# Kernel optimization log

Hardware: AMD Instinct MI355X
Metric: run time of the kernel (lower is better)

Reference implementation:

```python
import jax, jax.numpy as jnp
import numpy as np

H, B, D, C = 6, 512, 2048, 1000   # heads (5 ICs + backbone exit), batch, feat dim, classes
TAU = 0.5                          # confidence_threshold


def setup_inputs() -> dict:
    key = jax.random.key(0)
    k1, k2, k3, k4 = jax.random.split(key, 4)
    feats = jax.random.normal(k1, (H, B, D), dtype=jnp.float32)          # pooled reps at each exit
    W = jax.random.normal(k2, (H, D, C), dtype=jnp.float32) * 0.07       # per-head classifier weights
    b = jax.random.normal(k3, (H, C), dtype=jnp.float32) * 0.1
    y_true = jax.random.randint(k4, (B,), 0, C)
    return {"feats": feats, "W": W, "b": b, "y_true": y_true}


def reference(feats, W, b, y_true):
    # Per-head logits for every sample (vectorized replacement for the shrinking-batch loop).
    logits = jnp.einsum('hbd,hdc->hbc', feats, W) + b[:, None, :]        # [H, B, C]
    logp = jax.nn.log_softmax(logits, axis=-1)
    conf = jnp.exp(logp).max(axis=-1)                                    # [H, B] max softmax prob (prob_conf=True)

    # Early-exit routing: first head with conf >= TAU; else head with max confidence
    # (argmax returns the first occurrence, matching the strict '>' update in find_exit).
    exited = conf >= TAU                                                  # [H, B]
    any_exit = exited.any(axis=0)                                         # [B]
    first_exit = jnp.argmax(exited, axis=0)                               # [B] first True along heads
    best_conf = jnp.argmax(conf, axis=0)                                  # [B] fallback exit
    exit_idx = jnp.where(any_exit, first_exit, best_conf)                 # [B] == sample_exited_at

    # Gather the chosen head's logits per sample (vectorized masked-scatter of sample_outputs).
    outputs = jnp.take_along_axis(logits, exit_idx[None, :, None], axis=0)[0]   # [B, C]

    # criterion_ic: cross-entropy loss + accuracy on routed outputs
    out_logp = jax.nn.log_softmax(outputs, axis=-1)
    loss = -jnp.take_along_axis(out_logp, y_true[:, None], axis=1).mean()
    acc = (outputs.argmax(axis=-1) == y_true).astype(jnp.float32).mean()
    return outputs, exit_idx.astype(jnp.int32), loss, acc
```

## Files before the change

kernel.cpp:

```cpp
#include <hip/hip_runtime.h>
#include <math.h>

#define Hn 6
#define Bn 512
#define Dn 2048
#define Cn 1000
#define Cpad 1024
#define TAUv 0.5f
#define KSPLIT 4
#define KPER (Dn / KSPLIT)
#define KT 32
#define NIT (KPER / KT)
#define NKT (Dn / KT)

typedef unsigned int u32;
typedef unsigned short u16;
typedef __attribute__((ext_vector_type(8))) short short8;
typedef __attribute__((ext_vector_type(4))) float f32x4;

union FragU { u32 d[4]; short8 s; };

__device__ __forceinline__ u32 bf16_rne(float f) {
  const u32 u = __float_as_uint(f);
  return (u + 0x7FFFu + ((u >> 16) & 1u)) >> 16;
}
__device__ __forceinline__ u32 pack_rne2(float f0, float f1, float& r0, float& r1) {
  const u32 b0 = bf16_rne(f0), b1 = bf16_rne(f1);
  r0 = f0 - __uint_as_float(b0 << 16);
  r1 = f1 - __uint_as_float(b1 << 16);
  return b0 | (b1 << 16);
}

__device__ __forceinline__ void dma16(const void* g, void* l) {
  __builtin_amdgcn_global_load_lds(
      (const __attribute__((address_space(1))) u32*)g,
      (__attribute__((address_space(3))) u32*)l, 16, 0, 0);
}

__device__ __forceinline__ void pack8(const float* rr, uint4& hv, uint4& lv) {
  float x0, x1, x2, x3, y0, y1, y2, y3, d;
  hv.x = pack_rne2(rr[0], rr[1], x0, x1);
  hv.y = pack_rne2(rr[2], rr[3], x2, x3);
  hv.z = pack_rne2(rr[4], rr[5], y0, y1);
  hv.w = pack_rne2(rr[6], rr[7], y2, y3);
  lv.x = pack_rne2(x0, x1, d, d);
  lv.y = pack_rne2(x2, x3, d, d);
  lv.z = pack_rne2(y0, y1, d, d);
  lv.w = pack_rne2(y2, y3, d, d);
}

__global__ __launch_bounds__(256) void aconv_k(const float* __restrict__ feats,
                                               u16* __restrict__ Ah, u16* __restrict__ Al)
{
  const int t  = blockIdx.x;
  const int rg = blockIdx.y;
  const int h  = blockIdx.z;
  const int r0 = rg * 128;
  __shared__ float tile[128][33];
  const int tid = threadIdx.x;

#pragma unroll
  for (int i = 0; i < 4; ++i) {
    const int f = i * 256 + tid;
    const int r = f >> 3, q = f & 7;
    const float4 v = *(const float4*)(feats + ((size_t)(h * Bn + r0 + r) * Dn + t * 32 + q * 4));
    tile[r][q * 4 + 0] = v.x; tile[r][q * 4 + 1] = v.y;
    tile[r][q * 4 + 2] = v.z; tile[r][q * 4 + 3] = v.w;
  }
  __syncthreads();
#pragma unroll
  for (int i = 0; i < 2; ++i) {
    const int j = i * 256 + tid;
    const int c = j >> 7, r = j & 127;
    float rr[8];
#pragma unroll
    for (int e = 0; e < 8; ++e) rr[e] = tile[r][c * 8 + e];
    uint4 hv, lv;
    pack8(rr, hv, lv);
    const size_t o = (((size_t)(h * 64 + t) * 4 + c) * 512 + r0 + r);
    ((uint4*)Ah)[o] = hv;
    ((uint4*)Al)[o] = lv;
  }
}

__global__ __launch_bounds__(256) void bconv_k(const float* __restrict__ W,
                                               u16* __restrict__ Bh, u16* __restrict__ Bl)
{
  const int t  = blockIdx.x;
  const int ng = blockIdx.y;
  const int h  = blockIdx.z;
  const int n0 = ng * 128;
  __shared__ float tile[32][129];
  const int tid = threadIdx.x;

#pragma unroll
  for (int i = 0; i < 4; ++i) {
    const int f = i * 256 + tid;
    const int k = f >> 5, q = f & 31;
    const int n = n0 + q * 4;
    const float* src = W + ((size_t)h * Dn + t * 32 + k) * Cn;
    float4 v = make_float4(0.f, 0.f, 0.f, 0.f);
    if (n + 3 < Cn) {
      v = *(const float4*)(src + n);
    } else {
      if (n + 0 < Cn) v.x = src[n + 0];
      if (n + 1 < Cn) v.y = src[n + 1];
      if (n + 2 < Cn) v.z = src[n + 2];
      if (n + 3 < Cn) v.w = src[n + 3];
    }
    tile[k][q * 4 + 0] = v.x; tile[k][q * 4 + 1] = v.y;
    tile[k][q * 4 + 2] = v.z; tile[k][q * 4 + 3] = v.w;
  }
  __syncthreads();
#pragma unroll
  for (int i = 0; i < 2; ++i) {
    const int j = i * 256 + tid;
    const int c = j >> 7, n = j & 127;
    float rr[8];
#pragma unroll
    for (int e = 0; e < 8; ++e) rr[e] = tile[c * 8 + e][n];
    uint4 hv, lv;
    pack8(rr, hv, lv);
    const size_t o = (((size_t)(h * 64 + t) * 4 + c) * 1024 + n0 + n);
    ((uint4*)Bh)[o] = hv;
    ((uint4*)Bl)[o] = lv;
  }
}

__global__ __launch_bounds__(256, 3) void gemm_k(
    const u16* __restrict__ AhG, const u16* __restrict__ AlG,
    const u16* __restrict__ BhG, const u16* __restrict__ BlG,
    const float* __restrict__ bias, float* __restrict__ logits)
{
  const int h  = blockIdx.z >> 2;
  const int kz = blockIdx.z & 3;
  const int m0 = blockIdx.y * 128;
  const int n0 = blockIdx.x * 128;

  __shared__ __align__(16) short Ah[4][128][8];
  __shared__ __align__(16) short Al[4][128][8];
  __shared__ __align__(16) short Bh[4][128][8];
  __shared__ __align__(16) short Bl[4][128][8];

  const int t = threadIdx.x;
  const int lane = t & 63;
  const int w    = t >> 6;
  const int wm   = (w & 1) * 64;
  const int wn   = (w >> 1) * 64;
  const int fl   = lane & 15;
  const int fq   = lane >> 4;

  const u16* gmat = (w == 0) ? AhG : (w == 1) ? AlG : (w == 2) ? BhG : BlG;
  const int  R    = (w < 2) ? 512 : 1024;
  const int  row0 = (w < 2) ? m0 : n0;
  short* lbase = (w == 0) ? &Ah[0][0][0] : (w == 1) ? &Al[0][0][0]
               : (w == 2) ? &Bh[0][0][0] : &Bl[0][0][0];
  const uint4* g0 = (const uint4*)gmat
                  + ((size_t)(h * 64 + kz * NIT) * 4) * R + row0 + lane;

  f32x4 acc[4][4];
#pragma unroll
  for (int i = 0; i < 4; ++i)
#pragma unroll
    for (int j = 0; j < 4; ++j) acc[i][j] = (f32x4){0.f, 0.f, 0.f, 0.f};

  for (int it = 0; it < NIT; ++it) {
    const size_t ito = (size_t)(it * 4) * R;
#pragma unroll
    for (int c = 0; c < 4; ++c) {
      dma16(g0 + ito + (size_t)c * R,      lbase + (c * 128) * 8);
      dma16(g0 + ito + (size_t)c * R + 64, lbase + (c * 128 + 64) * 8);
    }
    __syncthreads();

    FragU ah[4], al[4];
#pragma unroll
    for (int mt = 0; mt < 4; ++mt) {
      const int m = wm + mt * 16 + fl;
      ah[mt].s = *(const short8*)(&Ah[fq][m][0]);
      al[mt].s = *(const short8*)(&Al[fq][m][0]);
    }
#pragma unroll
    for (int nt = 0; nt < 4; ++nt) {
      const int n = wn + nt * 16 + fl;
      FragU bh, bl;
      bh.s = *(const short8*)(&Bh[fq][n][0]);
      bl.s = *(const short8*)(&Bl[fq][n][0]);
#pragma unroll
      for (int mt = 0; mt < 4; ++mt) {
        acc[mt][nt] = __builtin_amdgcn_mfma_f32_16x16x32_bf16(ah[mt].s, bh.s, acc[mt][nt], 0, 0, 0);
        acc[mt][nt] = __builtin_amdgcn_mfma_f32_16x16x32_bf16(ah[mt].s, bl.s, acc[mt][nt], 0, 0, 0);
        acc[mt][nt] = __builtin_amdgcn_mfma_f32_16x16x32_bf16(al[mt].s, bh.s, acc[mt][nt], 0, 0, 0);
      }
    }
    __syncthreads();
  }

  float* part = logits + (size_t)kz * ((size_t)Hn * Bn * Cn);
#pragma unroll
  for (int nt = 0; nt < 4; ++nt) {
    const int col = n0 + wn + nt * 16 + fl;
    if (col >= Cn) continue;
    const float bv = (kz == 0) ? bias[(size_t)h * Cn + col] : 0.f;
#pragma unroll
    for (int mt = 0; mt < 4; ++mt) {
      const int rbase = m0 + wm + mt * 16 + fq * 4;
#pragma unroll
      for (int r = 0; r < 4; ++r)
        part[((size_t)h * Bn + rbase + r) * Cn + col] = acc[mt][nt][r] + bv;
    }
  }
}

__global__ __launch_bounds__(256) void conf_k(const float* __restrict__ logits,
                                              float* __restrict__ ms,
                                              float* __restrict__ ss,
                                              float* __restrict__ scalars)
{
  if (blockIdx.x == 0 && threadIdx.x == 0) { scalars[0] = 0.f; scalars[1] = 0.f; }
  const int w = threadIdx.x >> 6, lane = threadIdx.x & 63;
  const int r = blockIdx.x * 4 + w;
  const float* p = logits + (size_t)r * Cn;
  const size_t S = (size_t)Hn * Bn * Cn;

  float vv[16];
#pragma unroll
  for (int i = 0; i < 4; ++i) {
    const int c4 = i * 256 + lane * 4;
    if (c4 + 3 < Cn) {
      const float4 v0 = *(const float4*)(p + c4);
      const float4 v1 = *(const float4*)(p + S + c4);
      const float4 v2 = *(const float4*)(p + 2 * S + c4);
      const float4 v3 = *(const float4*)(p + 3 * S + c4);
      vv[4 * i + 0] = v0.x + v1.x + v2.x + v3.x;
      vv[4 * i + 1] = v0.y + v1.y + v2.y + v3.y;
      vv[4 * i + 2] = v0.z + v1.z + v2.z + v3.z;
      vv[4 * i + 3] = v0.w + v1.w + v2.w + v3.w;
    } else {
#pragma unroll
      for (int j = 0; j < 4; ++j) {
        const int c = c4 + j;
        vv[4 * i + j] = (c < Cn) ? p[c] + p[S + c] + p[2 * S + c] + p[3 * S + c] : -3.4e38f;
      }
    }
  }
  float m = -3.4e38f;
#pragma unroll
  for (int i = 0; i < 16; ++i) m = fmaxf(m, vv[i]);
#pragma unroll
  for (int off = 32; off >= 1; off >>= 1) m = fmaxf(m, __shfl_xor(m, off));
  float s = 0.f;
#pragma unroll
  for (int i = 0; i < 16; ++i) s += (vv[i] > -3.0e38f) ? expf(vv[i] - m) : 0.f;
#pragma unroll
  for (int off = 32; off >= 1; off >>= 1) s += __shfl_xor(s, off);
  if (lane == 0) { ms[r] = m; ss[r] = s; }
}

__global__ __launch_bounds__(256) void pick_k(
    const float* __restrict__ logits, const float* __restrict__ ms,
    const float* __restrict__ ss, const int* __restrict__ y,
    float* __restrict__ out, float* __restrict__ out_exit,
    float* __restrict__ scalars)
{
  const int b = blockIdx.x, t = threadIdx.x;
  const size_t S = (size_t)Hn * Bn * Cn;

  int first = -1, best = 0;
  float bestc = -3.4e38f;
#pragma unroll
  for (int h = 0; h < Hn; ++h) {
    const float c = 1.0f / ss[h * Bn + b];
    if (first < 0 && c >= TAUv) first = h;
    if (c > bestc) { bestc = c; best = h; }
  }
  const int ex = (first >= 0) ? first : best;
  const float* p = logits + ((size_t)ex * Bn + b) * Cn;

  const int c4 = t * 4;
  float vv[4] = {-3.4e38f, -3.4e38f, -3.4e38f, -3.4e38f};
  if (c4 + 3 < Cn) {
    const float4 v0 = *(const float4*)(p + c4);
    const float4 v1 = *(const float4*)(p + S + c4);
    const float4 v2 = *(const float4*)(p + 2 * S + c4);
    const float4 v3 = *(const float4*)(p + 3 * S + c4);
    vv[0] = v0.x + v1.x + v2.x + v3.x;
    vv[1] = v0.y + v1.y + v2.y + v3.y;
    vv[2] = v0.z + v1.z + v2.z + v3.z;
    vv[3] = v0.w + v1.w + v2.w + v3.w;
  }
  float vm = -3.4e38f; int im = 1 << 30;
#pragma unroll
  for (int j = 0; j < 4; ++j) {
    const int c = c4 + j;
    if (c < Cn) {
      out[(size_t)b * Cn + c] = vv[j];
      if (vv[j] > vm) { vm = vv[j]; im = c; }
    }
  }
  const int lane = t & 63, w = t >> 6;
#pragma unroll
  for (int off = 32; off >= 1; off >>= 1) {
    const float ov = __shfl_xor(vm, off);
    const int   oi = __shfl_xor(im, off);
    if (ov > vm || (ov == vm && oi < im)) { vm = ov; im = oi; }
  }
  __shared__ float rm[4]; __shared__ int ri[4];
  if (lane == 0) { rm[w] = vm; ri[w] = im; }
  __syncthreads();
  if (t == 0) {
    float bm = rm[0]; int bi = ri[0];
    for (int q = 1; q < 4; ++q)
      if (rm[q] > bm || (rm[q] == bm && ri[q] < bi)) { bm = rm[q]; bi = ri[q]; }
    const int yt = y[b];
    const float ryt = p[yt] + p[S + yt] + p[2 * S + yt] + p[3 * S + yt];
    const float lp = ryt - ms[ex * Bn + b] - logf(ss[ex * Bn + b]);
    out_exit[b] = (float)ex;
    atomicAdd(&scalars[0], -lp * (1.0f / (float)Bn));
    atomicAdd(&scalars[1], ((bi == yt) ? 1.f : 0.f) * (1.0f / (float)Bn));
  }
}

extern "C" void kernel_launch(void* const* d_in, const int* in_sizes, int n_in,
                              void* d_out, int out_size, void* d_ws, size_t ws_size,
                              hipStream_t stream) {
  const float* feats = (const float*)d_in[0];
  const float* W     = (const float*)d_in[1];
  const float* bias  = (const float*)d_in[2];
  const int*   y     = (const int*)d_in[3];
  float* out = (float*)d_out;

  float* logits = (float*)d_ws;
  float* ms     = logits + (size_t)KSPLIT * Hn * Bn * Cn;
  float* ss     = ms + Hn * Bn;
  u16*   AhG    = (u16*)(ss + Hn * Bn);
  u16*   AlG    = AhG + (size_t)Hn * Bn * Dn;
  u16*   BhG    = AlG + (size_t)Hn * Bn * Dn;
  u16*   BlG    = BhG + (size_t)Hn * Cpad * Dn;

  float* out_exit    = out + (size_t)Bn * Cn;
  float* out_scalars = out + (size_t)Bn * Cn + Bn;

  aconv_k<<<dim3(NKT, Bn / 128, Hn), 256, 0, stream>>>(feats, AhG, AlG);
  bconv_k<<<dim3(NKT, Cpad / 128, Hn), 256, 0, stream>>>(W, BhG, BlG);
  gemm_k<<<dim3(Cpad / 128, Bn / 128, Hn * KSPLIT), 256, 0, stream>>>(
      AhG, AlG, BhG, BlG, bias, logits);
  conf_k<<<(Hn * Bn) / 4, 256, 0, stream>>>(logits, ms, ss, out_scalars);
  pick_k<<<Bn, 256, 0, stream>>>(logits, ms, ss, y, out, out_exit, out_scalars);
}
```

Before: 198.2 us.

## Halve split-K and use 128x64 two-wave GEMM tiles

Split-K drops from 4 to 2, and the GEMM block shrinks to two waves covering a 128x64 output tile, each wave computing 64x64. Block count stays the same (16x4x12 versus 8x4x24) while the partial-sum buffers written by the GEMM and re-read by conf_k and pick_k are halved. The risk is fewer waves per block, with each wave now issuing three DMA loads per k-step and a longer K loop, which could hurt latency hiding.

```diff
diff --git a/kernel.cpp b/kernel.cpp
--- a/kernel.cpp
+++ b/kernel.cpp
@@ -7,7 +7,7 @@
 #define Cn 1000
 #define Cpad 1024
 #define TAUv 0.5f
-#define KSPLIT 4
+#define KSPLIT 2
 #define KPER (Dn / KSPLIT)
 #define KT 32
 #define NIT (KPER / KT)
@@ -127,36 +127,36 @@
   }
 }
 
-__global__ __launch_bounds__(256, 3) void gemm_k(
+__global__ __launch_bounds__(128, 3) void gemm_k(
     const u16* __restrict__ AhG, const u16* __restrict__ AlG,
     const u16* __restrict__ BhG, const u16* __restrict__ BlG,
     const float* __restrict__ bias, float* __restrict__ logits)
 {
-  const int h  = blockIdx.z >> 2;
-  const int kz = blockIdx.z & 3;
+  const int h  = blockIdx.z >> 1;
+  const int kz = blockIdx.z & 1;
   const int m0 = blockIdx.y * 128;
-  const int n0 = blockIdx.x * 128;
+  const int n0 = blockIdx.x * 64;
 
   __shared__ __align__(16) short Ah[4][128][8];
   __shared__ __align__(16) short Al[4][128][8];
-  __shared__ __align__(16) short Bh[4][128][8];
-  __shared__ __align__(16) short Bl[4][128][8];
+  __shared__ __align__(16) short Bh[4][64][8];
+  __shared__ __align__(16) short Bl[4][64][8];
 
   const int t = threadIdx.x;
   const int lane = t & 63;
   const int w    = t >> 6;
-  const int wm   = (w & 1) * 64;
-  const int wn   = (w >> 1) * 64;
+  const int wm   = w * 64;
   const int fl   = lane & 15;
   const int fq   = lane >> 4;
 
-  const u16* gmat = (w == 0) ? AhG : (w == 1) ? AlG : (w == 2) ? BhG : BlG;
-  const int  R    = (w < 2) ? 512 : 1024;
-  const int  row0 = (w < 2) ? m0 : n0;
-  short* lbase = (w == 0) ? &Ah[0][0][0] : (w == 1) ? &Al[0][0][0]
-               : (w == 2) ? &Bh[0][0][0] : &Bl[0][0][0];
-  const uint4* g0 = (const uint4*)gmat
-                  + ((size_t)(h * 64 + kz * NIT) * 4) * R + row0 + lane;
+  const u16* Ag = w ? AlG : AhG;
+  const u16* Bg = w ? BlG : BhG;
+  short* Ald = w ? &Al[0][0][0] : &Ah[0][0][0];
+  short* Bld = w ? &Bl[0][0][0] : &Bh[0][0][0];
+
+  const int kt0 = kz * NIT;
+  const uint4* gA = (const uint4*)Ag + ((size_t)(h * 64 + kt0) * 4) * 512 + m0 + lane;
+  const uint4* gB = (const uint4*)Bg + ((size_t)(h * 64 + kt0) * 4) * 1024 + n0 + lane;
 
   f32x4 acc[4][4];
 #pragma unroll
@@ -165,11 +165,13 @@
     for (int j = 0; j < 4; ++j) acc[i][j] = (f32x4){0.f, 0.f, 0.f, 0.f};
 
   for (int it = 0; it < NIT; ++it) {
-    const size_t ito = (size_t)(it * 4) * R;
 #pragma unroll
     for (int c = 0; c < 4; ++c) {
-      dma16(g0 + ito + (size_t)c * R,      lbase + (c * 128) * 8);
-      dma16(g0 + ito + (size_t)c * R + 64, lbase + (c * 128 + 64) * 8);
+      const size_t ao = (size_t)(it * 4 + c) * 512;
+      const size_t bo = (size_t)(it * 4 + c) * 1024;
+      dma16(gA + ao,      Ald + (c * 128) * 8);
+      dma16(gA + ao + 64, Ald + (c * 128 + 64) * 8);
+      dma16(gB + bo,      Bld + (c * 64) * 8);
     }
     __syncthreads();
 
@@ -182,7 +184,7 @@
     }
 #pragma unroll
     for (int nt = 0; nt < 4; ++nt) {
-      const int n = wn + nt * 16 + fl;
+      const int n = nt * 16 + fl;
       FragU bh, bl;
       bh.s = *(const short8*)(&Bh[fq][n][0]);
       bl.s = *(const short8*)(&Bl[fq][n][0]);
@@ -199,7 +201,7 @@
   float* part = logits + (size_t)kz * ((size_t)Hn * Bn * Cn);
 #pragma unroll
   for (int nt = 0; nt < 4; ++nt) {
-    const int col = n0 + wn + nt * 16 + fl;
+    const int col = n0 + nt * 16 + fl;
     if (col >= Cn) continue;
     const float bv = (kz == 0) ? bias[(size_t)h * Cn + col] : 0.f;
 #pragma unroll
@@ -230,17 +232,15 @@
     if (c4 + 3 < Cn) {
       const float4 v0 = *(const float4*)(p + c4);
       const float4 v1 = *(const float4*)(p + S + c4);
-      const float4 v2 = *(const float4*)(p + 2 * S + c4);
-      const float4 v3 = *(const float4*)(p + 3 * S + c4);
-      vv[4 * i + 0] = v0.x + v1.x + v2.x + v3.x;
-      vv[4 * i + 1] = v0.y + v1.y + v2.y + v3.y;
-      vv[4 * i + 2] = v0.z + v1.z + v2.z + v3.z;
-      vv[4 * i + 3] = v0.w + v1.w + v2.w + v3.w;
+      vv[4 * i + 0] = v0.x + v1.x;
+      vv[4 * i + 1] = v0.y + v1.y;
+      vv[4 * i + 2] = v0.z + v1.z;
+      vv[4 * i + 3] = v0.w + v1.w;
     } else {
 #pragma unroll
       for (int j = 0; j < 4; ++j) {
         const int c = c4 + j;
-        vv[4 * i + j] = (c < Cn) ? p[c] + p[S + c] + p[2 * S + c] + p[3 * S + c] : -3.4e38f;
+        vv[4 * i + j] = (c < Cn) ? p[c] + p[S + c] : -3.4e38f;
       }
     }
   }
@@ -282,12 +282,10 @@
   if (c4 + 3 < Cn) {
     const float4 v0 = *(const float4*)(p + c4);
     const float4 v1 = *(const float4*)(p + S + c4);
-    const float4 v2 = *(const float4*)(p + 2 * S + c4);
-    const float4 v3 = *(const float4*)(p + 3 * S + c4);
-    vv[0] = v0.x + v1.x + v2.x + v3.x;
-    vv[1] = v0.y + v1.y + v2.y + v3.y;
-    vv[2] = v0.z + v1.z + v2.z + v3.z;
-    vv[3] = v0.w + v1.w + v2.w + v3.w;
+    vv[0] = v0.x + v1.x;
+    vv[1] = v0.y + v1.y;
+    vv[2] = v0.z + v1.z;
+    vv[3] = v0.w + v1.w;
   }
   float vm = -3.4e38f; int im = 1 << 30;
 #pragma unroll
@@ -313,7 +311,7 @@
     for (int q = 1; q < 4; ++q)
       if (rm[q] > bm || (rm[q] == bm && ri[q] < bi)) { bm = rm[q]; bi = ri[q]; }
     const int yt = y[b];
-    const float ryt = p[yt] + p[S + yt] + p[2 * S + yt] + p[3 * S + yt];
+    const float ryt = p[yt] + p[S + yt];
     const float lp = ryt - ms[ex * Bn + b] - logf(ss[ex * Bn + b]);
     out_exit[b] = (float)ex;
     atomicAdd(&scalars[0], -lp * (1.0f / (float)Bn));
@@ -343,7 +341,7 @@
 
   aconv_k<<<dim3(NKT, Bn / 128, Hn), 256, 0, stream>>>(feats, AhG, AlG);
   bconv_k<<<dim3(NKT, Cpad / 128, Hn), 256, 0, stream>>>(W, BhG, BlG);
-  gemm_k<<<dim3(Cpad / 128, Bn / 128, Hn * KSPLIT), 256, 0, stream>>>(
+  gemm_k<<<dim3(Cpad / 64, Bn / 128, Hn * KSPLIT), 128, 0, stream>>>(
       AhG, AlG, BhG, BlG, bias, logits);
   conf_k<<<(Hn * Bn) / 4, 256, 0, stream>>>(logits, ms, ss, out_scalars);
   pick_k<<<Bn, 256, 0, stream>>>(logits, ms, ss, y, out, out_exit, out_scalars);
```

Measured after the change: 197.2 us. No clear change (-0.5%).
